# Kernel tuning notes

Hardware: AMD Instinct MI355X
Metric: run time of the kernel (lower is better)

The kernel has to match this reference:

```python
import jax, jax.numpy as jnp
import numpy as np

B, S, HID, NH, MAX_TOKENS = 2, 2048, 2048, 16, 2048
HD = HID // NH

def rotate_half(x):
    x1, x2 = x[..., :x.shape[-1] // 2], x[..., x.shape[-1] // 2:]
    return jnp.concatenate((-x2, x1), axis=-1)

def rope_tables():
    inv_freq = 1.0 / (10000.0 ** (jnp.arange(0, HD, 2, dtype=jnp.float32) / HD))
    t = jnp.arange(MAX_TOKENS, dtype=jnp.float32)
    freqs = jnp.outer(t, inv_freq)                       # [T, HD/2]
    emb = jnp.concatenate((freqs, freqs), axis=-1)       # [T, HD]
    return jnp.cos(emb), jnp.sin(emb)

def setup_inputs() -> dict:
    key = jax.random.key(0)
    ks = jax.random.split(key, 5)
    hidden_states = jax.random.normal(ks[0], (B, S, HID), dtype=jnp.float32)
    # additive causal mask [B, 1, S, S]: 0 on/below diag, large negative above
    neg = jnp.finfo(jnp.float32).min
    causal = jnp.where(jnp.tril(jnp.ones((S, S), dtype=bool)), 0.0, neg)
    attention_mask = jnp.broadcast_to(causal[None, None], (B, 1, S, S)).astype(jnp.float32)
    position_ids = jnp.broadcast_to(jnp.arange(S, dtype=jnp.int32), (B, S))
    scale = 1.0 / np.sqrt(HID)
    Wq = jax.random.normal(ks[1], (HID, HID), dtype=jnp.float32) * scale
    Wk = jax.random.normal(ks[2], (HID, HID), dtype=jnp.float32) * scale
    Wv = jax.random.normal(ks[3], (HID, HID), dtype=jnp.float32) * scale
    Wo = jax.random.normal(ks[4], (HID, HID), dtype=jnp.float32) * scale
    return {"hidden_states": hidden_states, "attention_mask": attention_mask,
            "position_ids": position_ids, "Wq": Wq, "Wk": Wk, "Wv": Wv, "Wo": Wo}

def reference(hidden_states, attention_mask, position_ids, Wq, Wk, Wv, Wo):
    b, s, _ = hidden_states.shape
    def proj(W):  # torch Linear: x @ W.T -> [b, H, s, hd]
        return (hidden_states @ W.T).reshape(b, s, NH, HD).transpose(0, 2, 1, 3)
    q, k, v = proj(Wq), proj(Wk), proj(Wv)
    cos_t, sin_t = rope_tables()
    cos = cos_t[position_ids][:, None]   # [b, 1, s, hd]
    sin = sin_t[position_ids][:, None]
    q = q * cos + rotate_half(q) * sin
    k = k * cos + rotate_half(k) * sin
    scores = jnp.einsum('bhqd,bhkd->bhqk', q, k) / np.sqrt(HD)
    scores = jnp.maximum(scores + attention_mask, jnp.finfo(scores.dtype).min)
    attn = jax.nn.softmax(scores.astype(jnp.float32), axis=-1).astype(q.dtype)
    out = jnp.einsum('bhqk,bhkd->bhqd', attn, v)
    out = out.transpose(0, 2, 1, 3).reshape(b, s, HID)
    return out @ Wo.T
```

## Files before the change

### kernel.cpp

```cpp
#include <hip/hip_runtime.h>

#define B_   2
#define S_   2048
#define HID_ 2048
#define NH_  16
#define HD_  128
#define MAXTOK_ 2048

typedef float  f32x4  __attribute__((ext_vector_type(4)));
typedef __bf16 bf16x8 __attribute__((ext_vector_type(8)));

__device__ __forceinline__ unsigned short f2bf(float f) {
  union { float fv; unsigned u; } v; v.fv = f;
  unsigned r = v.u + 0x7FFFu + ((v.u >> 16) & 1u);
  return (unsigned short)(r >> 16);
}
__device__ __forceinline__ float bf2f(unsigned short h) {
  union { unsigned u; float fv; } v; v.u = ((unsigned)h) << 16;
  return v.fv;
}

__device__ __forceinline__ void gload16(const void* g, void* lds) {
  __builtin_amdgcn_global_load_lds(
      (const __attribute__((address_space(1))) void*)g,
      (__attribute__((address_space(3))) void*)lds, 16, 0, 0);
}

#define H4_ (B_ * S_ * HID_ / 4)
#define W4_ (HID_ * HID_ / 4)
__global__ void cast_all(const float* __restrict__ h,  const float* __restrict__ wq,
                         const float* __restrict__ wk, const float* __restrict__ wv,
                         const float* __restrict__ wo,
                         unsigned short* __restrict__ xb,  unsigned short* __restrict__ wqb,
                         unsigned short* __restrict__ wkb, unsigned short* __restrict__ wvb,
                         unsigned short* __restrict__ wob) {
  const int total = H4_ + 4 * W4_;
  int i = blockIdx.x * blockDim.x + threadIdx.x;
  int stride = gridDim.x * blockDim.x;
  for (; i < total; i += stride) {
    const float* src; unsigned short* dst; int j;
    if (i < H4_) { src = h; dst = xb; j = i; }
    else {
      int k = i - H4_, wsel = k >> 20;
      j = k & (W4_ - 1);
      src = (wsel == 0) ? wq : (wsel == 1) ? wk : (wsel == 2) ? wv : wo;
      dst = (wsel == 0) ? wqb : (wsel == 1) ? wkb : (wsel == 2) ? wvb : wob;
    }
    float4 v = ((const float4*)src)[j];
    ushort4 o;
    o.x = f2bf(v.x); o.y = f2bf(v.y); o.z = f2bf(v.z); o.w = f2bf(v.w);
    ((ushort4*)dst)[j] = o;
  }
}

#define QKV_STG(gp, lp, rb) gload16((gp) + (size_t)(rb) * 2048, (lp) + (rb) * 64)

#define QKV_LOADA(Q) do { \
  _Pragma("unroll") \
  for (int mi_ = 0; mi_ < 2; ++mi_) { \
    const char* rp_ = (const char*)Acur + (size_t)((wm + (Q) * 32 + mi_ * 16 + rowq) * 128); \
    af[mi_][0] = *(const bf16x8*)(rp_ + cb0); \
    af[mi_][1] = *(const bf16x8*)(rp_ + cb1); \
  } } while (0)

#define QKV_LOADB() do { \
  _Pragma("unroll") \
  for (int ni_ = 0; ni_ < 3; ++ni_) { \
    const char* rp_ = (const char*)Bcur + (size_t)((wn + ni_ * 16 + rowq) * 128); \
    bfr[ni_][0] = *(const bf16x8*)(rp_ + cb0); \
    bfr[ni_][1] = *(const bf16x8*)(rp_ + cb1); \
  } } while (0)

#define QKV_MFMA(Q) do { \
  _Pragma("unroll") \
  for (int mi_ = 0; mi_ < 2; ++mi_) { \
    _Pragma("unroll") \
    for (int ni_ = 0; ni_ < 3; ++ni_) { \
      f32x4 c_ = acc[(Q) * 2 + mi_][ni_]; \
      c_ = __builtin_amdgcn_mfma_f32_16x16x32_bf16(af[mi_][0], bfr[ni_][0], c_, 0, 0, 0); \
      c_ = __builtin_amdgcn_mfma_f32_16x16x32_bf16(af[mi_][1], bfr[ni_][1], c_, 0, 0, 0); \
      acc[(Q) * 2 + mi_][ni_] = c_; \
    } } } while (0)

#define QKV_BAR    asm volatile("s_barrier" ::: "memory")
#define QKV_VMC4   asm volatile("s_waitcnt vmcnt(4)" ::: "memory")
#define QKV_VMC2   asm volatile("s_waitcnt vmcnt(2)" ::: "memory")
#define QKV_VMC0   asm volatile("s_waitcnt vmcnt(0)" ::: "memory")

__global__ __launch_bounds__(512, 2)
void gemm_qkv(const unsigned short* __restrict__ A,
              const unsigned short* __restrict__ Bw,
              unsigned short* __restrict__ Qb,
              unsigned short* __restrict__ Kb,
              unsigned short* __restrict__ Vtmp) {
  const int K = HID_;
  const int NT = K / 64;
  __shared__ __align__(16) unsigned short As[2][256 * 64];
  __shared__ __align__(16) unsigned short Bs[2][192 * 64];

  const int tid = threadIdx.x, lane = tid & 63, w = tid >> 6;
  const int n0 = blockIdx.x * 192, m0 = blockIdx.y * 256;
  const int wm = (w >> 2) * 128, wn = (w & 3) * 48;
  const int rowq = lane & 15, klane = lane >> 4;
  const int sw  = (rowq & 7) << 4;
  const int cb0 = (klane * 16) ^ sw;
  const int cb1 = ((klane + 4) * 16) ^ sw;
  const int srow = tid >> 3;
  const int dc8  = (tid & 7) * 8;
  const int scol = (((tid & 7) * 16) ^ ((srow & 7) << 4)) >> 1;

  const unsigned short* Ag = A  + (size_t)(m0 + srow) * K + scol;
  const unsigned short* Bg = Bw + (size_t)(n0 + srow) * K + scol;

  f32x4 acc[8][3];
#pragma unroll
  for (int i = 0; i < 8; ++i)
#pragma unroll
    for (int j = 0; j < 3; ++j)
#pragma unroll
      for (int r = 0; r < 4; ++r) acc[i][j][r] = 0.f;

  bf16x8 af[2][2], bfr[3][2];

  {
    unsigned short* Al = (unsigned short*)&As[0][0] + srow * 64 + dc8;
    unsigned short* Bl = (unsigned short*)&Bs[0][0] + srow * 64 + dc8;
    QKV_STG(Bg, Bl, 0); QKV_STG(Bg, Bl, 64); QKV_STG(Bg, Bl, 128);
    QKV_STG(Ag, Al, 0); QKV_STG(Ag, Al, 128);
    QKV_STG(Ag, Al, 64); QKV_STG(Ag, Al, 192);
  }
  QKV_VMC2;
  QKV_BAR;

  const unsigned short* Acur = &As[0][0];
  const unsigned short* Bcur = &Bs[0][0];
  unsigned short* Anx = (unsigned short*)&As[1][0];
  unsigned short* Bnx = (unsigned short*)&Bs[1][0];

  for (int t = 0; t < NT - 1; ++t) {
    const int kn = (t + 1) * 64;
    const unsigned short* Agk = Ag + kn;
    const unsigned short* Bgk = Bg + kn;
    unsigned short* Al = Anx + srow * 64 + dc8;
    unsigned short* Bl = Bnx + srow * 64 + dc8;

    QKV_LOADA(0); QKV_LOADB();
    QKV_STG(Bgk, Bl, 0); QKV_STG(Bgk, Bl, 64);
    QKV_BAR;
    __builtin_amdgcn_s_setprio(1); QKV_MFMA(0); __builtin_amdgcn_s_setprio(0);
    QKV_BAR;
    QKV_LOADA(1);
    QKV_STG(Bgk, Bl, 128); QKV_STG(Agk, Al, 0);
    QKV_BAR;
    __builtin_amdgcn_s_setprio(1); QKV_MFMA(1); __builtin_amdgcn_s_setprio(0);
    QKV_VMC4;
    QKV_BAR;
    QKV_LOADA(2);
    QKV_STG(Agk, Al, 128); QKV_STG(Agk, Al, 64);
    QKV_BAR;
    __builtin_amdgcn_s_setprio(1); QKV_MFMA(2); __builtin_amdgcn_s_setprio(0);
    QKV_BAR;
    QKV_LOADA(3);
    QKV_STG(Agk, Al, 192);
    QKV_BAR;
    __builtin_amdgcn_s_setprio(1); QKV_MFMA(3); __builtin_amdgcn_s_setprio(0);
    QKV_VMC2;
    QKV_BAR;

    { const unsigned short* tp = Acur; Acur = Anx; Anx = (unsigned short*)tp; }
    { const unsigned short* tp = Bcur; Bcur = Bnx; Bnx = (unsigned short*)tp; }
  }

  QKV_LOADA(0); QKV_LOADB();
  QKV_BAR;
  __builtin_amdgcn_s_setprio(1); QKV_MFMA(0); __builtin_amdgcn_s_setprio(0);
  QKV_BAR;
  QKV_LOADA(1);
  QKV_BAR;
  __builtin_amdgcn_s_setprio(1); QKV_MFMA(1); __builtin_amdgcn_s_setprio(0);
  QKV_VMC0;
  QKV_BAR;
  QKV_LOADA(2);
  QKV_BAR;
  __builtin_amdgcn_s_setprio(1); QKV_MFMA(2); __builtin_amdgcn_s_setprio(0);
  QKV_BAR;
  QKV_LOADA(3);
  __builtin_amdgcn_s_setprio(1); QKV_MFMA(3); __builtin_amdgcn_s_setprio(0);

  const int lr0 = klane * 4;
#pragma unroll
  for (int mi = 0; mi < 8; ++mi)
#pragma unroll
    for (int ni = 0; ni < 3; ++ni)
#pragma unroll
      for (int r = 0; r < 4; ++r) {
        int r_ = m0 + wm + mi * 16 + lr0 + r;
        int c_ = n0 + wn + ni * 16 + rowq;
        float v = acc[mi][ni][r];
        int b = r_ >> 11, s = r_ & 2047;
        int proj = c_ >> 11, cin = c_ & 2047;
        if (proj == 2) {
          Vtmp[(size_t)(b * S_ + s) * HID_ + cin] = f2bf(v);
        } else {
          int hh = cin >> 7, d = cin & 127;
          unsigned short* dst = (proj == 0) ? Qb : Kb;
          dst[(((size_t)(b * NH_ + hh) * S_ + s) * HD_) + d] = f2bf(v);
        }
      }
}

__global__ __launch_bounds__(256, 2)
void gemm_out(const unsigned short* __restrict__ A,
              const unsigned short* __restrict__ Bw,
              float* __restrict__ Cout) {
  const int N = HID_, K = HID_;
  __shared__ __align__(16) unsigned short As[128 * 32];
  __shared__ __align__(16) unsigned short Bs[128 * 32];
  const int tid = threadIdx.x, lane = tid & 63, w = tid >> 6;
  const int n0 = blockIdx.x * 128, m0 = blockIdx.y * 128;
  const int wm = (w & 1) * 64, wn = (w >> 1) * 64;
  const int rowq = lane & 15;
  const int klane = lane >> 4;
  const int ko = ((klane ^ ((rowq >> 1) & 3)) * 8);
  const int lr0 = klane * 4;

  f32x4 acc[4][4];
  for (int i = 0; i < 4; ++i)
    for (int j = 0; j < 4; ++j)
      for (int r = 0; r < 4; ++r) acc[i][j][r] = 0.f;

  for (int k0 = 0; k0 < K; k0 += 32) {
    __syncthreads();
    for (int c = 0; c < 2; ++c) {
      int chunk = (w * 2 + c) * 64 + lane;
      int row = chunk >> 2, cc = chunk & 3;
      int sc = (cc ^ ((row >> 1) & 3)) * 8;
      gload16(A + (size_t)(m0 + row) * K + k0 + sc, As + (w * 2 + c) * 512);
      gload16(Bw + (size_t)(n0 + row) * K + k0 + sc, Bs + (w * 2 + c) * 512);
    }
    __syncthreads();
    bf16x8 af[4], bfv[4];
    for (int i = 0; i < 4; ++i) {
      af[i]  = *(const bf16x8*)&As[(wm + i * 16 + rowq) * 32 + ko];
      bfv[i] = *(const bf16x8*)&Bs[(wn + i * 16 + rowq) * 32 + ko];
    }
    for (int mi = 0; mi < 4; ++mi)
      for (int ni = 0; ni < 4; ++ni)
        acc[mi][ni] = __builtin_amdgcn_mfma_f32_16x16x32_bf16(af[mi], bfv[ni], acc[mi][ni], 0, 0, 0);
  }

  for (int mi = 0; mi < 4; ++mi)
    for (int ni = 0; ni < 4; ++ni)
      for (int r = 0; r < 4; ++r) {
        int r_ = m0 + wm + mi * 16 + lr0 + r;
        int c_ = n0 + wn + ni * 16 + rowq;
        Cout[(size_t)r_ * N + c_] = acc[mi][ni][r];
      }
}

__global__ void rope_table(float2* __restrict__ tbl) {
  int i = blockIdx.x * blockDim.x + threadIdx.x;
  if (i >= MAXTOK_ * 64) return;
  int p = i >> 6, d = i & 63;
  float f = __expf(-(float)d * (9.210340371976184f / 64.f));
  float sn, cs;
  __sincosf((float)p * f, &sn, &cs);
  tbl[i] = make_float2(cs, sn);
}

#define QSCALE_ 0.12751744f
__global__ __launch_bounds__(256)
void rope_apply(unsigned short* __restrict__ Qb, unsigned short* __restrict__ Kb,
                const int* __restrict__ pos_ids, const float2* __restrict__ tbl) {
  int i = blockIdx.x * blockDim.x + threadIdx.x;
  int d = i & 63, bhs = i >> 6;
  int s = bhs & (S_ - 1);
  int b = bhs >> 15;
  int p = pos_ids[b * S_ + s];
  float2 cssn = tbl[p * 64 + d];
  size_t base = (size_t)bhs * HD_;
  {
    float x1 = bf2f(Qb[base + d]), x2 = bf2f(Qb[base + d + 64]);
    Qb[base + d]      = f2bf((x1 * cssn.x - x2 * cssn.y) * QSCALE_);
    Qb[base + d + 64] = f2bf((x2 * cssn.x + x1 * cssn.y) * QSCALE_);
  }
  {
    float x1 = bf2f(Kb[base + d]), x2 = bf2f(Kb[base + d + 64]);
    Kb[base + d]      = f2bf(x1 * cssn.x - x2 * cssn.y);
    Kb[base + d + 64] = f2bf(x2 * cssn.x + x1 * cssn.y);
  }
}

__global__ __launch_bounds__(256)
void transpose_v(const unsigned short* __restrict__ Vin,
                 unsigned short* __restrict__ Vt) {
  __shared__ unsigned short t[64 * 66];
  const int s0 = blockIdx.x * 64, d0 = blockIdx.y * 64, bh = blockIdx.z;
  const int b = bh >> 4, h = bh & 15;
  for (int it = 0; it < 16; ++it) {
    int lin = it * 256 + threadIdx.x;
    int sl = lin >> 6, dl = lin & 63;
    t[sl * 66 + dl] = Vin[(size_t)(b * S_ + s0 + sl) * HID_ + h * HD_ + d0 + dl];
  }
  __syncthreads();
  for (int it = 0; it < 16; ++it) {
    int lin = it * 256 + threadIdx.x;
    int dl = lin >> 6, sl = lin & 63;
    Vt[((size_t)bh * HD_ + d0 + dl) * S_ + s0 + sl] = t[sl * 66 + dl];
  }
}

#define KS_LD 136
#define VS_LD 72
#define PS_LD 72
__global__ __launch_bounds__(256, 2)
void attn_fused(const unsigned short* __restrict__ Qb,
                const unsigned short* __restrict__ Kb,
                const unsigned short* __restrict__ Vt,
                unsigned short* __restrict__ Ob) {
  __shared__ __align__(16) unsigned short Ks[64 * KS_LD];
  __shared__ __align__(16) unsigned short Vts[128 * VS_LD];
  __shared__ __align__(16) unsigned short Ps[4 * 16 * PS_LD];

  const int tid = threadIdx.x, lane = tid & 63, w = tid >> 6;
  const int bh = blockIdx.x;
  const int qt = (gridDim.y - 1) - blockIdx.y;
  const int q0 = qt * 64;
  const int b = bh >> 4, h = bh & 15;
  const int rowq = lane & 15;
  const int koff = (lane >> 4) * 8;
  const int lr0 = (lane >> 4) * 4;
  const size_t qkbase = (size_t)bh * (S_ * HD_);
  const size_t vbase  = (size_t)bh * (HD_ * S_);

  bf16x8 qf0, qf1, qf2, qf3;
  {
    const unsigned short* qrow = Qb + qkbase + (size_t)(q0 + w * 16 + rowq) * HD_;
    qf0 = *(const bf16x8*)(qrow + 0 * 32 + koff);
    qf1 = *(const bf16x8*)(qrow + 1 * 32 + koff);
    qf2 = *(const bf16x8*)(qrow + 2 * 32 + koff);
    qf3 = *(const bf16x8*)(qrow + 3 * 32 + koff);
  }

  const int krow = tid >> 4, kcol = (tid & 15) * 8;
  const int vrow = tid >> 3, vcol = (tid & 7) * 8;
  const unsigned short* kptr = Kb + qkbase + (size_t)krow * HD_ + kcol;
  const unsigned short* vptr = Vt + vbase + (size_t)vrow * S_ + vcol;

  f32x4 oacc[8];
  for (int i = 0; i < 8; ++i)
    for (int r = 0; r < 4; ++r) oacc[i][r] = 0.f;
  float m_r[4] = {-3e38f, -3e38f, -3e38f, -3e38f};
  float l_r[4] = {0.f, 0.f, 0.f, 0.f};

  const int nkt = qt + 1;

  float4 k0, k1, k2, k3, v0, v1, v2, v3;
  k0 = *(const float4*)(kptr + 0 * 16 * HD_);
  k1 = *(const float4*)(kptr + 1 * 16 * HD_);
  k2 = *(const float4*)(kptr + 2 * 16 * HD_);
  k3 = *(const float4*)(kptr + 3 * 16 * HD_);
  v0 = *(const float4*)(vptr + 0 * 32 * S_);
  v1 = *(const float4*)(vptr + 1 * 32 * S_);
  v2 = *(const float4*)(vptr + 2 * 32 * S_);
  v3 = *(const float4*)(vptr + 3 * 32 * S_);

  for (int kt = 0; kt < nkt; ++kt) {
    __syncthreads();
    *(float4*)&Ks[(krow + 0 * 16) * KS_LD + kcol] = k0;
    *(float4*)&Ks[(krow + 1 * 16) * KS_LD + kcol] = k1;
    *(float4*)&Ks[(krow + 2 * 16) * KS_LD + kcol] = k2;
    *(float4*)&Ks[(krow + 3 * 16) * KS_LD + kcol] = k3;
    *(float4*)&Vts[(vrow + 0 * 32) * VS_LD + vcol] = v0;
    *(float4*)&Vts[(vrow + 1 * 32) * VS_LD + vcol] = v1;
    *(float4*)&Vts[(vrow + 2 * 32) * VS_LD + vcol] = v2;
    *(float4*)&Vts[(vrow + 3 * 32) * VS_LD + vcol] = v3;
    if (kt + 1 < nkt) {
      const unsigned short* kp = kptr + (size_t)(kt + 1) * 64 * HD_;
      k0 = *(const float4*)(kp + 0 * 16 * HD_);
      k1 = *(const float4*)(kp + 1 * 16 * HD_);
      k2 = *(const float4*)(kp + 2 * 16 * HD_);
      k3 = *(const float4*)(kp + 3 * 16 * HD_);
    }
    __syncthreads();

    f32x4 sacc[4];
    for (int n = 0; n < 4; ++n)
      for (int r = 0; r < 4; ++r) sacc[n][r] = 0.f;
#pragma unroll
    for (int n = 0; n < 4; ++n) {
      const unsigned short* krow_p = &Ks[(n * 16 + rowq) * KS_LD + koff];
      sacc[n] = __builtin_amdgcn_mfma_f32_16x16x32_bf16(qf0, *(const bf16x8*)(krow_p + 0 * 32), sacc[n], 0, 0, 0);
      sacc[n] = __builtin_amdgcn_mfma_f32_16x16x32_bf16(qf1, *(const bf16x8*)(krow_p + 1 * 32), sacc[n], 0, 0, 0);
      sacc[n] = __builtin_amdgcn_mfma_f32_16x16x32_bf16(qf2, *(const bf16x8*)(krow_p + 2 * 32), sacc[n], 0, 0, 0);
      sacc[n] = __builtin_amdgcn_mfma_f32_16x16x32_bf16(qf3, *(const bf16x8*)(krow_p + 3 * 32), sacc[n], 0, 0, 0);
    }

    float tmax[4] = {-3e38f, -3e38f, -3e38f, -3e38f};
    if (kt == qt) {
      for (int n = 0; n < 4; ++n) {
        int col = n * 16 + rowq;
        for (int r = 0; r < 4; ++r) {
          int row = w * 16 + lr0 + r;
          float x = (col <= row) ? sacc[n][r] : -1e30f;
          sacc[n][r] = x;
          tmax[r] = fmaxf(tmax[r], x);
        }
      }
    } else {
      for (int n = 0; n < 4; ++n)
        for (int r = 0; r < 4; ++r)
          tmax[r] = fmaxf(tmax[r], sacc[n][r]);
    }
    for (int off = 1; off < 16; off <<= 1)
      for (int r = 0; r < 4; ++r) tmax[r] = fmaxf(tmax[r], __shfl_xor(tmax[r], off));
    float alpha[4];
    for (int r = 0; r < 4; ++r) {
      float mn = fmaxf(m_r[r], tmax[r]);
      alpha[r] = __builtin_amdgcn_exp2f(m_r[r] - mn);
      m_r[r] = mn;
    }
    float rs[4] = {0.f, 0.f, 0.f, 0.f};
    for (int n = 0; n < 4; ++n)
      for (int r = 0; r < 4; ++r) {
        float p = __builtin_amdgcn_exp2f(sacc[n][r] - m_r[r]);
        sacc[n][r] = p;
        rs[r] += p;
      }
    for (int off = 1; off < 16; off <<= 1)
      for (int r = 0; r < 4; ++r) rs[r] += __shfl_xor(rs[r], off);
    for (int r = 0; r < 4; ++r) l_r[r] = l_r[r] * alpha[r] + rs[r];
    for (int nd = 0; nd < 8; ++nd)
      for (int r = 0; r < 4; ++r) oacc[nd][r] *= alpha[r];

    if (kt + 1 < nkt) {
      const unsigned short* vp = vptr + (size_t)(kt + 1) * 64;
      v0 = *(const float4*)(vp + 0 * 32 * S_);
      v1 = *(const float4*)(vp + 1 * 32 * S_);
      v2 = *(const float4*)(vp + 2 * 32 * S_);
      v3 = *(const float4*)(vp + 3 * 32 * S_);
    }

    unsigned short* pw = &Ps[w * 16 * PS_LD];
    for (int n = 0; n < 4; ++n)
      for (int r = 0; r < 4; ++r)
        pw[(lr0 + r) * PS_LD + n * 16 + rowq] = f2bf(sacc[n][r]);

#pragma unroll
    for (int t2 = 0; t2 < 2; ++t2) {
      bf16x8 pa = *(const bf16x8*)&pw[rowq * PS_LD + t2 * 32 + koff];
      for (int nd = 0; nd < 8; ++nd) {
        bf16x8 vb = *(const bf16x8*)&Vts[(nd * 16 + rowq) * VS_LD + t2 * 32 + koff];
        oacc[nd] = __builtin_amdgcn_mfma_f32_16x16x32_bf16(pa, vb, oacc[nd], 0, 0, 0);
      }
    }
  }

  float linv[4];
  for (int r = 0; r < 4; ++r) linv[r] = __builtin_amdgcn_rcpf(l_r[r]);
  for (int nd = 0; nd < 8; ++nd) {
    int col = h * HD_ + nd * 16 + rowq;
    for (int r = 0; r < 4; ++r) {
      int row = q0 + w * 16 + lr0 + r;
      Ob[(size_t)(b * S_ + row) * HID_ + col] = f2bf(oacc[nd][r] * linv[r]);
    }
  }
}

extern "C" void kernel_launch(void* const* d_in, const int* in_sizes, int n_in,
                              void* d_out, int out_size, void* d_ws, size_t ws_size,
                              hipStream_t stream) {
  (void)in_sizes; (void)n_in; (void)out_size; (void)ws_size;
  const float* hidden = (const float*)d_in[0];
  const int* pos = (const int*)d_in[2];
  const float* Wq = (const float*)d_in[3];
  const float* Wk = (const float*)d_in[4];
  const float* Wv = (const float*)d_in[5];
  const float* Wo = (const float*)d_in[6];
  float* out = (float*)d_out;

  char* ws = (char*)d_ws;
  unsigned short* Xb   = (unsigned short*)(ws);
  unsigned short* Wqb  = (unsigned short*)(ws + 16777216);
  unsigned short* Wkb  = (unsigned short*)(ws + 25165824);
  unsigned short* Wvb  = (unsigned short*)(ws + 33554432);
  unsigned short* Wob  = (unsigned short*)(ws + 41943040);
  unsigned short* Qb   = (unsigned short*)(ws + 50331648);
  unsigned short* Kb   = (unsigned short*)(ws + 67108864);
  unsigned short* Vtmp = (unsigned short*)(ws + 83886080);
  unsigned short* Vtb  = (unsigned short*)(ws + 100663296);
  unsigned short* Ob   = Xb;
  float2* tbl          = (float2*)ws;

  cast_all<<<2048, 256, 0, stream>>>(hidden, Wq, Wk, Wv, Wo, Xb, Wqb, Wkb, Wvb, Wob);

  dim3 gq(3 * HID_ / 192, (B_ * S_) / 256);
  gemm_qkv<<<gq, 512, 0, stream>>>(Xb, Wqb, Qb, Kb, Vtmp);

  rope_table<<<(MAXTOK_ * 64) / 256, 256, 0, stream>>>(tbl);
  rope_apply<<<(B_ * NH_ * S_ * 64) / 256, 256, 0, stream>>>(Qb, Kb, pos, tbl);

  dim3 tg(S_ / 64, HD_ / 64, B_ * NH_);
  transpose_v<<<tg, 256, 0, stream>>>(Vtmp, Vtb);

  dim3 ag(B_ * NH_, S_ / 64);
  attn_fused<<<ag, 256, 0, stream>>>(Qb, Kb, Vtb, Ob);

  dim3 go(HID_ / 128, (B_ * S_) / 128);
  gemm_out<<<go, 256, 0, stream>>>(Ob, Wob, out);
}
```

Before: 399.9 us.

## Pipeline output GEMM with double-buffered LDS and vectorize RoPE and V transpose

Rewrites the output projection GEMM to use 256x128 tiles, 512 threads and BK=64 with double-buffered LDS. It reuses the QKV GEMM's staged-load and barrier macros so global loads overlap with MFMA work, and raises wave priority around the MFMA phases. The RoPE apply and V transpose kernels are separately vectorized to 16-byte loads and stores, cutting the thread count and memory transactions. The larger LDS footprint (96KB per block) and register use may limit occupancy below the declared two blocks per CU.

```diff
diff --git a/kernel.cpp b/kernel.cpp
--- a/kernel.cpp
+++ b/kernel.cpp
@@ -9,6 +9,7 @@
 
 typedef float  f32x4  __attribute__((ext_vector_type(4)));
 typedef __bf16 bf16x8 __attribute__((ext_vector_type(8)));
+typedef unsigned short u16x8 __attribute__((ext_vector_type(8)));
 
 __device__ __forceinline__ unsigned short f2bf(float f) {
   union { float fv; unsigned u; } v; v.fv = f;
@@ -209,48 +210,129 @@
       }
 }
 
-__global__ __launch_bounds__(256, 2)
+#define OUT_LOADB() do { \
+  _Pragma("unroll") \
+  for (int ni_ = 0; ni_ < 2; ++ni_) { \
+    const char* rp_ = (const char*)Bcur + (size_t)((wn + ni_ * 16 + rowq) * 128); \
+    bfr[ni_][0] = *(const bf16x8*)(rp_ + cb0); \
+    bfr[ni_][1] = *(const bf16x8*)(rp_ + cb1); \
+  } } while (0)
+
+#define OUT_MFMA(Q) do { \
+  _Pragma("unroll") \
+  for (int mi_ = 0; mi_ < 2; ++mi_) { \
+    _Pragma("unroll") \
+    for (int ni_ = 0; ni_ < 2; ++ni_) { \
+      f32x4 c_ = acc[(Q) * 2 + mi_][ni_]; \
+      c_ = __builtin_amdgcn_mfma_f32_16x16x32_bf16(af[mi_][0], bfr[ni_][0], c_, 0, 0, 0); \
+      c_ = __builtin_amdgcn_mfma_f32_16x16x32_bf16(af[mi_][1], bfr[ni_][1], c_, 0, 0, 0); \
+      acc[(Q) * 2 + mi_][ni_] = c_; \
+    } } } while (0)
+
+__global__ __launch_bounds__(512, 2)
 void gemm_out(const unsigned short* __restrict__ A,
               const unsigned short* __restrict__ Bw,
               float* __restrict__ Cout) {
-  const int N = HID_, K = HID_;
-  __shared__ __align__(16) unsigned short As[128 * 32];
-  __shared__ __align__(16) unsigned short Bs[128 * 32];
+  const int K = HID_, N = HID_;
+  const int NT = K / 64;
+  __shared__ __align__(16) unsigned short As[2][256 * 64];
+  __shared__ __align__(16) unsigned short Bs[2][128 * 64];
+
   const int tid = threadIdx.x, lane = tid & 63, w = tid >> 6;
-  const int n0 = blockIdx.x * 128, m0 = blockIdx.y * 128;
-  const int wm = (w & 1) * 64, wn = (w >> 1) * 64;
-  const int rowq = lane & 15;
-  const int klane = lane >> 4;
-  const int ko = ((klane ^ ((rowq >> 1) & 3)) * 8);
+  const int n0 = blockIdx.x * 128, m0 = blockIdx.y * 256;
+  const int wm = (w >> 2) * 128, wn = (w & 3) * 32;
+  const int rowq = lane & 15, klane = lane >> 4;
+  const int sw  = (rowq & 7) << 4;
+  const int cb0 = (klane * 16) ^ sw;
+  const int cb1 = ((klane + 4) * 16) ^ sw;
+  const int srow = tid >> 3;
+  const int dc8  = (tid & 7) * 8;
+  const int scol = (((tid & 7) * 16) ^ ((srow & 7) << 4)) >> 1;
+
+  const unsigned short* Ag = A  + (size_t)(m0 + srow) * K + scol;
+  const unsigned short* Bg = Bw + (size_t)(n0 + srow) * K + scol;
+
+  f32x4 acc[8][2];
+#pragma unroll
+  for (int i = 0; i < 8; ++i)
+#pragma unroll
+    for (int j = 0; j < 2; ++j)
+#pragma unroll
+      for (int r = 0; r < 4; ++r) acc[i][j][r] = 0.f;
+
+  bf16x8 af[2][2], bfr[2][2];
+
+  {
+    unsigned short* Al = (unsigned short*)&As[0][0] + srow * 64 + dc8;
+    unsigned short* Bl = (unsigned short*)&Bs[0][0] + srow * 64 + dc8;
+    QKV_STG(Bg, Bl, 0); QKV_STG(Bg, Bl, 64);
+    QKV_STG(Ag, Al, 0); QKV_STG(Ag, Al, 128);
+    QKV_STG(Ag, Al, 64); QKV_STG(Ag, Al, 192);
+  }
+  QKV_VMC2;
+  QKV_BAR;
+
+  const unsigned short* Acur = &As[0][0];
+  const unsigned short* Bcur = &Bs[0][0];
+  unsigned short* Anx = (unsigned short*)&As[1][0];
+  unsigned short* Bnx = (unsigned short*)&Bs[1][0];
+
+  for (int t = 0; t < NT - 1; ++t) {
+    const int kn = (t + 1) * 64;
+    const unsigned short* Agk = Ag + kn;
+    const unsigned short* Bgk = Bg + kn;
+    unsigned short* Al = Anx + srow * 64 + dc8;
+    unsigned short* Bl = Bnx + srow * 64 + dc8;
+
+    QKV_LOADA(0); OUT_LOADB();
+    QKV_STG(Bgk, Bl, 0); QKV_STG(Bgk, Bl, 64);
+    QKV_BAR;
+    __builtin_amdgcn_s_setprio(1); OUT_MFMA(0); __builtin_amdgcn_s_setprio(0);
+    QKV_BAR;
+    QKV_LOADA(1);
+    QKV_STG(Agk, Al, 0); QKV_STG(Agk, Al, 128);
+    QKV_BAR;
+    __builtin_amdgcn_s_setprio(1); OUT_MFMA(1); __builtin_amdgcn_s_setprio(0);
+    QKV_VMC4;
+    QKV_BAR;
+    QKV_LOADA(2);
+    QKV_STG(Agk, Al, 64);
+    QKV_BAR;
+    __builtin_amdgcn_s_setprio(1); OUT_MFMA(2); __builtin_amdgcn_s_setprio(0);
+    QKV_BAR;
+    QKV_LOADA(3);
+    QKV_STG(Agk, Al, 192);
+    QKV_BAR;
+    __builtin_amdgcn_s_setprio(1); OUT_MFMA(3); __builtin_amdgcn_s_setprio(0);
+    QKV_VMC2;
+    QKV_BAR;
+
+    { const unsigned short* tp = Acur; Acur = Anx; Anx = (unsigned short*)tp; }
+    { const unsigned short* tp = Bcur; Bcur = Bnx; Bnx = (unsigned short*)tp; }
+  }
+
+  QKV_LOADA(0); OUT_LOADB();
+  QKV_BAR;
+  __builtin_amdgcn_s_setprio(1); OUT_MFMA(0); __builtin_amdgcn_s_setprio(0);
+  QKV_BAR;
+  QKV_LOADA(1);
+  QKV_BAR;
+  __builtin_amdgcn_s_setprio(1); OUT_MFMA(1); __builtin_amdgcn_s_setprio(0);
+  QKV_VMC0;
+  QKV_BAR;
+  QKV_LOADA(2);
+  QKV_BAR;
+  __builtin_amdgcn_s_setprio(1); OUT_MFMA(2); __builtin_amdgcn_s_setprio(0);
+  QKV_BAR;
+  QKV_LOADA(3);
+  __builtin_amdgcn_s_setprio(1); OUT_MFMA(3); __builtin_amdgcn_s_setprio(0);
+
   const int lr0 = klane * 4;
-
-  f32x4 acc[4][4];
-  for (int i = 0; i < 4; ++i)
-    for (int j = 0; j < 4; ++j)
-      for (int r = 0; r < 4; ++r) acc[i][j][r] = 0.f;
-
-  for (int k0 = 0; k0 < K; k0 += 32) {
-    __syncthreads();
-    for (int c = 0; c < 2; ++c) {
-      int chunk = (w * 2 + c) * 64 + lane;
-      int row = chunk >> 2, cc = chunk & 3;
-      int sc = (cc ^ ((row >> 1) & 3)) * 8;
-      gload16(A + (size_t)(m0 + row) * K + k0 + sc, As + (w * 2 + c) * 512);
-      gload16(Bw + (size_t)(n0 + row) * K + k0 + sc, Bs + (w * 2 + c) * 512);
-    }
-    __syncthreads();
-    bf16x8 af[4], bfv[4];
-    for (int i = 0; i < 4; ++i) {
-      af[i]  = *(const bf16x8*)&As[(wm + i * 16 + rowq) * 32 + ko];
-      bfv[i] = *(const bf16x8*)&Bs[(wn + i * 16 + rowq) * 32 + ko];
-    }
-    for (int mi = 0; mi < 4; ++mi)
-      for (int ni = 0; ni < 4; ++ni)
-        acc[mi][ni] = __builtin_amdgcn_mfma_f32_16x16x32_bf16(af[mi], bfv[ni], acc[mi][ni], 0, 0, 0);
-  }
-
-  for (int mi = 0; mi < 4; ++mi)
-    for (int ni = 0; ni < 4; ++ni)
+#pragma unroll
+  for (int mi = 0; mi < 8; ++mi)
+#pragma unroll
+    for (int ni = 0; ni < 2; ++ni)
+#pragma unroll
       for (int r = 0; r < 4; ++r) {
         int r_ = m0 + wm + mi * 16 + lr0 + r;
         int c_ = n0 + wn + ni * 16 + rowq;
@@ -273,40 +355,67 @@
 void rope_apply(unsigned short* __restrict__ Qb, unsigned short* __restrict__ Kb,
                 const int* __restrict__ pos_ids, const float2* __restrict__ tbl) {
   int i = blockIdx.x * blockDim.x + threadIdx.x;
-  int d = i & 63, bhs = i >> 6;
+  int t8 = i & 7, bhs = i >> 3;
   int s = bhs & (S_ - 1);
   int b = bhs >> 15;
+  int d0 = t8 * 8;
   int p = pos_ids[b * S_ + s];
-  float2 cssn = tbl[p * 64 + d];
-  size_t base = (size_t)bhs * HD_;
+  const float2* tp = tbl + p * 64 + d0;
+  float cs[8], sn[8];
+#pragma unroll
+  for (int j = 0; j < 8; ++j) { float2 c2 = tp[j]; cs[j] = c2.x; sn[j] = c2.y; }
+  size_t base = (size_t)bhs * HD_ + d0;
   {
-    float x1 = bf2f(Qb[base + d]), x2 = bf2f(Qb[base + d + 64]);
-    Qb[base + d]      = f2bf((x1 * cssn.x - x2 * cssn.y) * QSCALE_);
-    Qb[base + d + 64] = f2bf((x2 * cssn.x + x1 * cssn.y) * QSCALE_);
+    u16x8 x1 = *(const u16x8*)(Qb + base);
+    u16x8 x2 = *(const u16x8*)(Qb + base + 64);
+    u16x8 o1, o2;
+#pragma unroll
+    for (int j = 0; j < 8; ++j) {
+      float a = bf2f(x1[j]), bb = bf2f(x2[j]);
+      o1[j] = f2bf((a * cs[j] - bb * sn[j]) * QSCALE_);
+      o2[j] = f2bf((bb * cs[j] + a * sn[j]) * QSCALE_);
+    }
+    *(u16x8*)(Qb + base) = o1;
+    *(u16x8*)(Qb + base + 64) = o2;
   }
   {
-    float x1 = bf2f(Kb[base + d]), x2 = bf2f(Kb[base + d + 64]);
-    Kb[base + d]      = f2bf(x1 * cssn.x - x2 * cssn.y);
-    Kb[base + d + 64] = f2bf(x2 * cssn.x + x1 * cssn.y);
+    u16x8 x1 = *(const u16x8*)(Kb + base);
+    u16x8 x2 = *(const u16x8*)(Kb + base + 64);
+    u16x8 o1, o2;
+#pragma unroll
+    for (int j = 0; j < 8; ++j) {
+      float a = bf2f(x1[j]), bb = bf2f(x2[j]);
+      o1[j] = f2bf(a * cs[j] - bb * sn[j]);
+      o2[j] = f2bf(bb * cs[j] + a * sn[j]);
+    }
+    *(u16x8*)(Kb + base) = o1;
+    *(u16x8*)(Kb + base + 64) = o2;
   }
 }
 
 __global__ __launch_bounds__(256)
 void transpose_v(const unsigned short* __restrict__ Vin,
                  unsigned short* __restrict__ Vt) {
-  __shared__ unsigned short t[64 * 66];
+  __shared__ __align__(16) unsigned short t[64 * 72];
   const int s0 = blockIdx.x * 64, d0 = blockIdx.y * 64, bh = blockIdx.z;
   const int b = bh >> 4, h = bh & 15;
-  for (int it = 0; it < 16; ++it) {
-    int lin = it * 256 + threadIdx.x;
-    int sl = lin >> 6, dl = lin & 63;
-    t[sl * 66 + dl] = Vin[(size_t)(b * S_ + s0 + sl) * HID_ + h * HD_ + d0 + dl];
+  const int tid = threadIdx.x;
+#pragma unroll
+  for (int it = 0; it < 2; ++it) {
+    int chunk = it * 256 + tid;
+    int sl = chunk >> 3, dc = (chunk & 7) * 8;
+    u16x8 v = *(const u16x8*)&Vin[(size_t)(b * S_ + s0 + sl) * HID_ + h * HD_ + d0 + dc];
+    *(u16x8*)&t[sl * 72 + dc] = v;
   }
   __syncthreads();
-  for (int it = 0; it < 16; ++it) {
-    int lin = it * 256 + threadIdx.x;
-    int dl = lin >> 6, sl = lin & 63;
-    Vt[((size_t)bh * HD_ + d0 + dl) * S_ + s0 + sl] = t[sl * 66 + dl];
+#pragma unroll
+  for (int it = 0; it < 2; ++it) {
+    int lin = it * 256 + tid;
+    int dl = lin & 63, sq = (lin >> 6) * 8;
+    u16x8 v;
+#pragma unroll
+    for (int j = 0; j < 8; ++j) v[j] = t[(sq + j) * 72 + dl];
+    *(u16x8*)&Vt[((size_t)bh * HD_ + d0 + dl) * S_ + s0 + sq] = v;
   }
 }
 
@@ -498,7 +607,7 @@
   gemm_qkv<<<gq, 512, 0, stream>>>(Xb, Wqb, Qb, Kb, Vtmp);
 
   rope_table<<<(MAXTOK_ * 64) / 256, 256, 0, stream>>>(tbl);
-  rope_apply<<<(B_ * NH_ * S_ * 64) / 256, 256, 0, stream>>>(Qb, Kb, pos, tbl);
+  rope_apply<<<(B_ * NH_ * S_ * 8) / 256, 256, 0, stream>>>(Qb, Kb, pos, tbl);
 
   dim3 tg(S_ / 64, HD_ / 64, B_ * NH_);
   transpose_v<<<tg, 256, 0, stream>>>(Vtmp, Vtb);
@@ -506,6 +615,6 @@
   dim3 ag(B_ * NH_, S_ / 64);
   attn_fused<<<ag, 256, 0, stream>>>(Qb, Kb, Vtb, Ob);
 
-  dim3 go(HID_ / 128, (B_ * S_) / 128);
-  gemm_out<<<go, 256, 0, stream>>>(Ob, Wob, out);
-}
+  dim3 go(HID_ / 128, (B_ * S_) / 256);
+  gemm_out<<<go, 512, 0, stream>>>(Ob, Wob, out);
+}
```

New measurement: 407.9 us. Within noise of the previous version (+2.0%).
